# Performance work log

Measured on AMD Instinct MI355X. Metric: run time of the kernel, lower is better.

## Reference

```python
import jax, jax.numpy as jnp
import numpy as np

# dims
N, E, B, T = 1024, 8192, 4, 8          # nodes, edges, batch, time steps
IN, HID, H, NCLASS = 64, 64, 4, 7      # in_dim, nhidden, heads, nclass
K = N - NCLASS + 1                     # output-head conv width
NEG, EPS = 0.2, 1e-5


def setup_inputs() -> dict:
    key = jax.random.key(0)
    ks = jax.random.split(key, 24)
    p = lambda i, shape: jax.random.normal(ks[i], shape, jnp.float32) * 0.05
    inputs = jax.random.normal(ks[0], (B, IN, T, N), jnp.float32)
    src = jax.random.randint(ks[1], (E,), 0, N, jnp.int32)
    dst = jnp.repeat(jnp.arange(N, dtype=jnp.int32), E // N)  # every node has in-degree 8
    return {
        "inputs": inputs, "src": src, "dst": dst,
        "W0": p(2, (H * HID, IN)), "al0": p(3, (H, HID)), "ar0": p(4, (H, HID)),
        "W1": p(5, (H * HID, H * HID)), "al1": p(6, (H, HID)), "ar1": p(7, (H, HID)),
        "W2": p(8, (H * 1, H * HID)), "al2": p(9, (H, 1)), "ar2": p(10, (H, 1)),
        "Wres2": p(11, (H * 1, H * HID)),
        # Outputlayer
        "tc1_w": p(12, (H, H, T)), "tc1_b": p(13, (H,)),
        "ln1_g": jnp.ones((N, H), jnp.float32), "ln1_b": jnp.zeros((N, H), jnp.float32),
        "tc2_w": p(14, (1, H)), "tc2_b": p(15, (1,)),
        "ln2_g": jnp.ones((N, 1), jnp.float32), "ln2_b": jnp.zeros((N, 1), jnp.float32),
        "fc_w": p(16, (K,)), "fc_b": p(17, (1,)),
    }


def _gat_conv(h, src, dst, W, al, ar, res=None, act=None):
    # h: (N,B,T,F) -> feat: (N,B,T,H,D)
    heads, d = al.shape
    feat = (h @ W.T).reshape(N, B, T, heads, d)
    el = jnp.einsum('nbthd,hd->nbth', feat, al)
    er = jnp.einsum('nbthd,hd->nbth', feat, ar)
    e = jax.nn.leaky_relu(el[src] + er[dst], NEG)           # (E,B,T,H)
    emax = jax.ops.segment_max(e, dst, num_segments=N)
    ex = jnp.exp(e - emax[dst])
    den = jax.ops.segment_sum(ex, dst, num_segments=N)
    a = ex / den[dst]                                        # edge softmax over incoming edges
    out = jax.ops.segment_sum(feat[src] * a[..., None], dst, num_segments=N)  # (N,B,T,H,D)
    if res is not None:
        out = out + res
    if act is not None:
        out = act(out)
    return out


def reference(inputs, src, dst,
              W0, al0, ar0, W1, al1, ar1, W2, al2, ar2, Wres2,
              tc1_w, tc1_b, ln1_g, ln1_b, tc2_w, tc2_b, ln2_g, ln2_b, fc_w, fc_b):
    # (B,IN,T,N) -> (N,B,T,IN) : transpose(0,3).transpose(1,3)
    h = jnp.transpose(inputs.astype(jnp.float32), (3, 0, 2, 1))
    h1 = _gat_conv(h, src, dst, W0, al0, ar0, act=jax.nn.elu).reshape(N, B, T, H * HID)
    h2 = _gat_conv(h1, src, dst, W1, al1, ar1,
                   res=h1.reshape(N, B, T, H, HID), act=jax.nn.elu).reshape(N, B, T, H * HID)
    res2 = (h2 @ Wres2.T).reshape(N, B, T, H, 1)
    o = _gat_conv(h2, src, dst, W2, al2, ar2, res=res2)      # (N,B,T,H,1)
    # transpose(1,3).transpose(0,3).squeeze(-1) -> (B,H,T,N)
    x = jnp.transpose(o[..., 0], (1, 3, 2, 0))

    # Outputlayer
    # tconv1: Conv2d(H->H, kernel (T,1)) collapses time -> (B,H,N)
    x1 = jnp.einsum('oht,bhtn->bon', tc1_w, x) + tc1_b[None, :, None]
    # ln1: LayerNorm over (N,H) of (B,1,N,H)
    z = jnp.transpose(x1, (0, 2, 1))                          # (B,N,H)
    mu = z.mean(axis=(1, 2), keepdims=True)
    var = z.var(axis=(1, 2), keepdims=True)
    z = (z - mu) / jnp.sqrt(var + EPS) * ln1_g + ln1_b
    x1 = jnp.transpose(z, (0, 2, 1))                          # (B,H,N)
    # tconv2: 1x1 conv H->1 -> (B,1,N)
    x2 = jnp.einsum('oh,bhn->bon', tc2_w, x1) + tc2_b[None, :, None]
    # ln2: LayerNorm over (N,1)
    mu = x2.mean(axis=2, keepdims=True)
    var = x2.var(axis=2, keepdims=True)
    x2 = (x2 - mu) / jnp.sqrt(var + EPS) * ln2_g[:, 0] + ln2_b[:, 0]
    # fc: Conv2d(1->1, kernel (1,K)) sliding over nodes -> (B,NCLASS)
    xc = x2[:, :, None, :]                                    # (B,1,1,N) NCHW
    w = fc_w[None, None, None, :]                             # (1,1,1,K) OIHW
    out = jax.lax.conv_general_dilated(xc, w, (1, 1), 'VALID') + fc_b[None, :, None, None]
    return out[:, 0, 0, :]                                    # (B, NCLASS)
```

## Files before the change

kernel.cpp:

```cpp
#include <hip/hip_runtime.h>
#include <math.h>

#define NEGS 0.2f
#define EPSF 1e-5f

typedef short s16x8 __attribute__((ext_vector_type(8)));
typedef float f32x4 __attribute__((ext_vector_type(4)));

__device__ __forceinline__ float b2f(unsigned short u) {
  union { unsigned int i; float f; } v; v.i = ((unsigned int)u) << 16; return v.f;
}
__device__ __forceinline__ unsigned short f2b(float f) {
  union { float f; unsigned int i; } v; v.f = f;
  unsigned int x = v.i;
  return (unsigned short)((x + 0x7fffu + ((x >> 16) & 1u)) >> 16);
}

__device__ __forceinline__ float block_reduce256(float v, float* red) {
  #pragma unroll
  for (int o = 32; o > 0; o >>= 1) v += __shfl_down(v, o);
  __syncthreads();
  if ((threadIdx.x & 63) == 0) red[threadIdx.x >> 6] = v;
  __syncthreads();
  return red[0] + red[1] + red[2] + red[3];
}

__global__ __launch_bounds__(256) void k_cvt(
    const float* __restrict__ inp, const float* __restrict__ W0,
    const float* __restrict__ W1, unsigned short* __restrict__ Xb,
    unsigned short* __restrict__ W0b, unsigned short* __restrict__ W1b)
{
  __shared__ float L[64][65];
  const int tid = threadIdx.x;
  if (blockIdx.x >= 512) {
    const int j = (blockIdx.x - 512) * 256 + tid;
    W0b[j] = f2b(W0[j]);
    float4 w4 = *(const float4*)&W1[j*4];
    ushort4 o4; o4.x = f2b(w4.x); o4.y = f2b(w4.y); o4.z = f2b(w4.z); o4.w = f2b(w4.w);
    *(ushort4*)&W1b[j*4] = o4;
    return;
  }
  const int blk = blockIdx.x;
  const int n0 = (blk & 15) * 64;
  const int t  = (blk >> 4) & 7;
  const int b  = blk >> 7;
  const int nn = tid & 63, ch0 = tid >> 6;
  #pragma unroll
  for (int ch = ch0; ch < 64; ch += 4)
    L[ch][nn] = inp[((size_t)(b*64 + ch)*8 + t)*1024 + n0 + nn];
  __syncthreads();
  const int r = tid >> 2, ck = tid & 3;
  s16x8 o0, o1;
  #pragma unroll
  for (int i = 0; i < 8; ++i) o0[i] = (short)f2b(L[ck*16 + i][r]);
  #pragma unroll
  for (int i = 0; i < 8; ++i) o1[i] = (short)f2b(L[ck*16 + 8 + i][r]);
  const int row = (n0 + r)*32 + b*8 + t;
  *(s16x8*)&Xb[(size_t)row*64 + ck*16]     = o0;
  *(s16x8*)&Xb[(size_t)row*64 + ck*16 + 8] = o1;
}

template<int KD>
__global__ __launch_bounds__(256) void k_feat_mfma(
    const unsigned short* __restrict__ X, const unsigned short* __restrict__ Wb,
    const float* __restrict__ al, const float* __restrict__ ar,
    unsigned short* __restrict__ feat, float* __restrict__ el, float* __restrict__ er)
{
  __shared__ __align__(16) unsigned short Lb[64*256];
  const int tid  = threadIdx.x;
  const int w    = tid >> 6;
  const int lane = tid & 63;
  const int n16  = lane & 15;
  const int q    = lane >> 4;
  const int r0   = blockIdx.x * 64;

  f32x4 acc[4][4];
  #pragma unroll
  for (int rt = 0; rt < 4; ++rt)
    #pragma unroll
    for (int ct = 0; ct < 4; ++ct) acc[rt][ct] = (f32x4){0.f,0.f,0.f,0.f};

  #pragma unroll
  for (int kc = 0; kc < KD/32; ++kc) {
    s16x8 af[4], bf[4];
    #pragma unroll
    for (int rt = 0; rt < 4; ++rt)
      af[rt] = *(const s16x8*)&X[(size_t)(r0 + rt*16 + n16)*KD + kc*32 + q*8];
    #pragma unroll
    for (int ct = 0; ct < 4; ++ct)
      bf[ct] = *(const s16x8*)&Wb[(size_t)((w*4 + ct)*16 + n16)*KD + kc*32 + q*8];
    #pragma unroll
    for (int rt = 0; rt < 4; ++rt)
      #pragma unroll
      for (int ct = 0; ct < 4; ++ct)
        acc[rt][ct] = __builtin_amdgcn_mfma_f32_16x16x32_bf16(af[rt], bf[ct], acc[rt][ct], 0, 0, 0);
  }

  float alv[4], arv[4];
  #pragma unroll
  for (int ct = 0; ct < 4; ++ct) {
    alv[ct] = al[w*64 + ct*16 + n16];
    arv[ct] = ar[w*64 + ct*16 + n16];
  }
  #pragma unroll
  for (int rt = 0; rt < 4; ++rt) {
    #pragma unroll
    for (int reg = 0; reg < 4; ++reg) {
      float pl = acc[rt][0][reg]*alv[0] + acc[rt][1][reg]*alv[1]
               + acc[rt][2][reg]*alv[2] + acc[rt][3][reg]*alv[3];
      float pr = acc[rt][0][reg]*arv[0] + acc[rt][1][reg]*arv[1]
               + acc[rt][2][reg]*arv[2] + acc[rt][3][reg]*arv[3];
      #pragma unroll
      for (int o = 1; o < 16; o <<= 1) { pl += __shfl_xor(pl, o); pr += __shfl_xor(pr, o); }
      if (n16 == 0) {
        int r = r0 + rt*16 + q*4 + reg;
        el[r*4 + w] = pl;
        er[r*4 + w] = pr;
      }
    }
  }

  #pragma unroll
  for (int rt = 0; rt < 4; ++rt)
    #pragma unroll
    for (int ct = 0; ct < 4; ++ct)
      #pragma unroll
      for (int reg = 0; reg < 4; ++reg)
        Lb[(rt*16 + q*4 + reg)*256 + w*64 + ct*16 + n16] = f2b(acc[rt][ct][reg]);
  __syncthreads();
  #pragma unroll
  for (int i = 0; i < 8; ++i) {
    int u = tid + i*256;
    int row = u >> 5, off = (u & 31) * 8;
    *(s16x8*)&feat[(size_t)(r0 + row)*256 + off] = *(const s16x8*)&Lb[row*256 + off];
  }
}

__global__ __launch_bounds__(256) void k_agg0_feat1(
    const unsigned short* __restrict__ feat0, const float* __restrict__ el0,
    const float* __restrict__ er0, const int* __restrict__ src,
    const unsigned short* __restrict__ W1b, const float* __restrict__ al,
    const float* __restrict__ ar, unsigned short* __restrict__ h1b,
    unsigned short* __restrict__ feat1, float* __restrict__ el1, float* __restrict__ er1)
{
  __shared__ float wsm[8][4][8][4];
  __shared__ int   ssm[8];
  __shared__ __align__(16) unsigned short smbuf[32*264];
  unsigned short (*At)[264] = (unsigned short(*)[264])smbuf;
  unsigned short *Lb = smbuf;
  const int tid = threadIdx.x;
  const int n   = blockIdx.x;
  if (tid < 8) ssm[tid] = src[n*8 + tid];
  __syncthreads();
  if (tid < 128) {
    const int h = tid & 3, t = (tid >> 2) & 7, b = tid >> 5;
    const int rn = n*32 + b*8 + t;
    const float erv = er0[rn*4 + h];
    float e[8]; float m = -1e30f;
    #pragma unroll
    for (int j = 0; j < 8; ++j) {
      float v = el0[(ssm[j]*32 + b*8 + t)*4 + h] + erv;
      v = v >= 0.f ? v : NEGS * v;
      e[j] = v; m = fmaxf(m, v);
    }
    float den = 0.f;
    #pragma unroll
    for (int j = 0; j < 8; ++j) { e[j] = __expf(e[j] - m); den += e[j]; }
    const float inv = 1.f / den;
    #pragma unroll
    for (int j = 0; j < 8; ++j) wsm[j][b][t][h] = e[j] * inv;
  }
  __syncthreads();
  {
    const int hw2 = tid >> 5;
    const int l5  = tid & 31;
    const int c0  = l5 * 8;
    const int hh  = l5 >> 3;
    #pragma unroll 1
    for (int pass = 0; pass < 4; ++pass) {
      const int row = pass*8 + hw2;
      const int bb = row >> 3, tt = row & 7;
      float a[8] = {0.f,0.f,0.f,0.f,0.f,0.f,0.f,0.f};
      #pragma unroll
      for (int j = 0; j < 8; ++j) {
        const int rs = ssm[j]*32 + row;
        s16x8 v = *(const s16x8*)&feat0[(size_t)rs*256 + c0];
        const float wj = wsm[j][bb][tt][hh];
        #pragma unroll
        for (int i = 0; i < 8; ++i) a[i] = fmaf(wj, b2f((unsigned short)v[i]), a[i]);
      }
      s16x8 o;
      #pragma unroll
      for (int i = 0; i < 8; ++i) {
        float x = a[i] > 0.f ? a[i] : expm1f(a[i]);
        o[i] = (short)f2b(x);
      }
      *(s16x8*)&At[row][c0] = o;
      *(s16x8*)&h1b[(size_t)(n*32 + row)*256 + c0] = o;
    }
  }
  __syncthreads();
  const int w    = tid >> 6;
  const int lane = tid & 63;
  const int n16  = lane & 15;
  const int q    = lane >> 4;
  const int r0   = n * 32;
  f32x4 acc[2][4];
  #pragma unroll
  for (int rt = 0; rt < 2; ++rt)
    #pragma unroll
    for (int ct = 0; ct < 4; ++ct) acc[rt][ct] = (f32x4){0.f,0.f,0.f,0.f};
  #pragma unroll
  for (int kc = 0; kc < 8; ++kc) {
    s16x8 af[2], bf[4];
    #pragma unroll
    for (int rt = 0; rt < 2; ++rt)
      af[rt] = *(const s16x8*)&At[rt*16 + n16][kc*32 + q*8];
    #pragma unroll
    for (int ct = 0; ct < 4; ++ct)
      bf[ct] = *(const s16x8*)&W1b[(size_t)((w*4 + ct)*16 + n16)*256 + kc*32 + q*8];
    #pragma unroll
    for (int rt = 0; rt < 2; ++rt)
      #pragma unroll
      for (int ct = 0; ct < 4; ++ct)
        acc[rt][ct] = __builtin_amdgcn_mfma_f32_16x16x32_bf16(af[rt], bf[ct], acc[rt][ct], 0, 0, 0);
  }
  float alv[4], arv[4];
  #pragma unroll
  for (int ct = 0; ct < 4; ++ct) {
    alv[ct] = al[w*64 + ct*16 + n16];
    arv[ct] = ar[w*64 + ct*16 + n16];
  }
  #pragma unroll
  for (int rt = 0; rt < 2; ++rt) {
    #pragma unroll
    for (int reg = 0; reg < 4; ++reg) {
      float pl = acc[rt][0][reg]*alv[0] + acc[rt][1][reg]*alv[1]
               + acc[rt][2][reg]*alv[2] + acc[rt][3][reg]*alv[3];
      float pr = acc[rt][0][reg]*arv[0] + acc[rt][1][reg]*arv[1]
               + acc[rt][2][reg]*arv[2] + acc[rt][3][reg]*arv[3];
      #pragma unroll
      for (int o = 1; o < 16; o <<= 1) { pl += __shfl_xor(pl, o); pr += __shfl_xor(pr, o); }
      if (n16 == 0) {
        int r = r0 + rt*16 + q*4 + reg;
        el1[r*4 + w] = pl;
        er1[r*4 + w] = pr;
      }
    }
  }
  __syncthreads();
  #pragma unroll
  for (int rt = 0; rt < 2; ++rt)
    #pragma unroll
    for (int ct = 0; ct < 4; ++ct)
      #pragma unroll
      for (int reg = 0; reg < 4; ++reg)
        Lb[(rt*16 + q*4 + reg)*256 + w*64 + ct*16 + n16] = f2b(acc[rt][ct][reg]);
  __syncthreads();
  #pragma unroll
  for (int i = 0; i < 4; ++i) {
    int u = tid + i*256;
    int row = u >> 5, off = (u & 31) * 8;
    *(s16x8*)&feat1[(size_t)(r0 + row)*256 + off] = *(const s16x8*)&Lb[row*256 + off];
  }
}

__global__ __launch_bounds__(256) void k_agg1_proj(
    const unsigned short* __restrict__ feat1, const float* __restrict__ el,
    const float* __restrict__ er, const int* __restrict__ src,
    const unsigned short* __restrict__ h1b, const float* __restrict__ W2,
    const float* __restrict__ Wres2, float* __restrict__ feat2, float* __restrict__ res2)
{
  __shared__ float wsm[8][4][8][4];
  __shared__ int   ssm[8];
  __shared__ __align__(16) float Wp[8][256];
  const int tid = threadIdx.x;
  const int n   = blockIdx.x;
  if (tid < 8) ssm[tid] = src[n*8 + tid];
  for (int j2 = tid; j2 < 2048; j2 += 256) {
    int o = j2 >> 8, k = j2 & 255;
    Wp[o][k] = (o < 4) ? W2[o*256 + k] : Wres2[(o-4)*256 + k];
  }
  __syncthreads();
  if (tid < 128) {
    const int h = tid & 3, t = (tid >> 2) & 7, b = tid >> 5;
    const int rn = n*32 + b*8 + t;
    const float erv = er[rn*4 + h];
    float e[8]; float m = -1e30f;
    #pragma unroll
    for (int j = 0; j < 8; ++j) {
      float v = el[(ssm[j]*32 + b*8 + t)*4 + h] + erv;
      v = v >= 0.f ? v : NEGS * v;
      e[j] = v; m = fmaxf(m, v);
    }
    float den = 0.f;
    #pragma unroll
    for (int j = 0; j < 8; ++j) { e[j] = __expf(e[j] - m); den += e[j]; }
    const float inv = 1.f / den;
    #pragma unroll
    for (int j = 0; j < 8; ++j) wsm[j][b][t][h] = e[j] * inv;
  }
  __syncthreads();
  const int hw2 = tid >> 5;
  const int l5  = tid & 31;
  const int c0  = l5 * 8;
  const int hh  = l5 >> 3;
  #pragma unroll 1
  for (int pass = 0; pass < 4; ++pass) {
    const int row = pass*8 + hw2;
    const int bb = row >> 3, tt = row & 7;
    const int rn = n*32 + row;
    float a[8] = {0.f,0.f,0.f,0.f,0.f,0.f,0.f,0.f};
    #pragma unroll
    for (int j = 0; j < 8; ++j) {
      const int rs = ssm[j]*32 + row;
      s16x8 v = *(const s16x8*)&feat1[(size_t)rs*256 + c0];
      const float wj = wsm[j][bb][tt][hh];
      #pragma unroll
      for (int i = 0; i < 8; ++i) a[i] = fmaf(wj, b2f((unsigned short)v[i]), a[i]);
    }
    s16x8 rr = *(const s16x8*)&h1b[(size_t)rn*256 + c0];
    #pragma unroll
    for (int i = 0; i < 8; ++i) {
      float x = a[i] + b2f((unsigned short)rr[i]);
      a[i] = x > 0.f ? x : expm1f(x);
    }
    #pragma unroll
    for (int o = 0; o < 8; ++o) {
      float4 wa = *(const float4*)&Wp[o][c0];
      float4 wb = *(const float4*)&Wp[o][c0 + 4];
      float p = a[0]*wa.x + a[1]*wa.y + a[2]*wa.z + a[3]*wa.w
              + a[4]*wb.x + a[5]*wb.y + a[6]*wb.z + a[7]*wb.w;
      #pragma unroll
      for (int off = 1; off < 32; off <<= 1) p += __shfl_xor(p, off);
      if (l5 == 0) {
        if (o < 4) feat2[rn*4 + o] = p;
        else       res2[rn*4 + (o-4)] = p;
      }
    }
  }
}

__global__ __launch_bounds__(128) void k_agg2(
    const float* __restrict__ feat2, const float* __restrict__ res2,
    const int* __restrict__ src, const float* __restrict__ al2,
    const float* __restrict__ ar2, const float* __restrict__ tc1w,
    const float* __restrict__ tc1b, float* __restrict__ x1)
{
  __shared__ float os[4][8][4];
  const int n = blockIdx.x;
  const int tid = threadIdx.x;
  const int b = tid >> 5, t = (tid >> 2) & 7, h = tid & 3;
  const int rn = n*32 + b*8 + t;
  const float av = al2[h], rv = ar2[h];
  const float erv = feat2[rn*4 + h] * rv;
  float f[8], e[8]; float m = -1e30f;
  #pragma unroll
  for (int j = 0; j < 8; ++j) {
    int s_ = src[n*8 + j];
    f[j] = feat2[(s_*32 + b*8 + t)*4 + h];
    float v = f[j]*av + erv;
    v = v >= 0.f ? v : NEGS * v;
    e[j] = v; m = fmaxf(m, v);
  }
  float den = 0.f, num = 0.f;
  #pragma unroll
  for (int j = 0; j < 8; ++j) { float ex = __expf(e[j]-m); den += ex; num = fmaf(ex, f[j], num); }
  os[b][t][h] = num/den + res2[rn*4 + h];
  __syncthreads();
  if (tid < 16) {
    int b2 = tid >> 2, o2 = tid & 3;
    float acc = tc1b[o2];
    #pragma unroll
    for (int hh = 0; hh < 4; ++hh)
      #pragma unroll
      for (int tt = 0; tt < 8; ++tt)
        acc = fmaf(tc1w[(o2*4 + hh)*8 + tt], os[b2][tt][hh], acc);
    x1[(b2*4 + o2)*1024 + n] = acc;
  }
}

__global__ __launch_bounds__(256) void k_final(
    const float* __restrict__ x1, const float* __restrict__ ln1g,
    const float* __restrict__ ln1b, const float* __restrict__ tc2w,
    const float* __restrict__ tc2b, const float* __restrict__ ln2g,
    const float* __restrict__ ln2b, const float* __restrict__ fcw,
    const float* __restrict__ fcb, float* __restrict__ out)
{
  __shared__ float red[4];
  __shared__ float x2s[1024];
  const int b = blockIdx.x;
  const int tid = threadIdx.x;
  float s = 0.f, q = 0.f;
  for (int j = tid; j < 4096; j += 256) {
    float v = x1[b*4096 + j];
    s += v; q += v*v;
  }
  float S = block_reduce256(s, red);
  float Q = block_reduce256(q, red);
  float mu  = S * (1.f/4096.f);
  float var = Q * (1.f/4096.f) - mu*mu;
  float inv = rsqrtf(var + EPSF);
  float tb = tc2b[0];
  float s2 = 0.f, q2 = 0.f;
  for (int nn = tid; nn < 1024; nn += 256) {
    float acc = tb;
    #pragma unroll
    for (int h = 0; h < 4; ++h) {
      float z = (x1[b*4096 + h*1024 + nn] - mu) * inv * ln1g[nn*4 + h] + ln1b[nn*4 + h];
      acc = fmaf(tc2w[h], z, acc);
    }
    x2s[nn] = acc;
    s2 += acc; q2 += acc*acc;
  }
  float S2 = block_reduce256(s2, red);
  float Q2 = block_reduce256(q2, red);
  float mu2  = S2 * (1.f/1024.f);
  float inv2 = rsqrtf(Q2 * (1.f/1024.f) - mu2*mu2 + EPSF);
  __syncthreads();
  for (int nn = tid; nn < 1024; nn += 256)
    x2s[nn] = (x2s[nn] - mu2) * inv2 * ln2g[nn] + ln2b[nn];
  __syncthreads();
  for (int c = 0; c < 7; ++c) {
    float p = 0.f;
    for (int k = tid; k < 1018; k += 256) p = fmaf(x2s[c + k], fcw[k], p);
    float P = block_reduce256(p, red);
    if (tid == 0) out[b*7 + c] = P + fcb[0];
  }
}

extern "C" void kernel_launch(void* const* d_in, const int* in_sizes, int n_in,
                              void* d_out, int out_size, void* d_ws, size_t ws_size,
                              hipStream_t stream)
{
  const float* inp  = (const float*)d_in[0];
  const int*   src  = (const int*)  d_in[1];
  const float* W0   = (const float*)d_in[3];
  const float* al0  = (const float*)d_in[4];
  const float* ar0  = (const float*)d_in[5];
  const float* W1   = (const float*)d_in[6];
  const float* al1  = (const float*)d_in[7];
  const float* ar1  = (const float*)d_in[8];
  const float* W2   = (const float*)d_in[9];
  const float* al2  = (const float*)d_in[10];
  const float* ar2  = (const float*)d_in[11];
  const float* Wr2  = (const float*)d_in[12];
  const float* tc1w = (const float*)d_in[13];
  const float* tc1b = (const float*)d_in[14];
  const float* ln1g = (const float*)d_in[15];
  const float* ln1b = (const float*)d_in[16];
  const float* tc2w = (const float*)d_in[17];
  const float* tc2b = (const float*)d_in[18];
  const float* ln2g = (const float*)d_in[19];
  const float* ln2b = (const float*)d_in[20];
  const float* fcw  = (const float*)d_in[21];
  const float* fcb  = (const float*)d_in[22];
  float* out = (float*)d_out;

  unsigned short* Xb     = (unsigned short*)d_ws;
  unsigned short* W0b    = Xb     + 2097152;
  unsigned short* W1b    = W0b    + 16384;
  unsigned short* featb0 = W1b    + 65536;
  unsigned short* featb1 = featb0 + 8388608;
  unsigned short* h1b    = featb1 + 8388608;
  float* el0   = (float*)(h1b + 8388608);
  float* er0   = el0   + 131072;
  float* el1   = er0   + 131072;
  float* er1   = el1   + 131072;
  float* feat2 = er1   + 131072;
  float* res2  = feat2 + 131072;
  float* x1    = res2  + 131072;

  k_cvt<<<dim3(576), dim3(256), 0, stream>>>(inp, W0, W1, Xb, W0b, W1b);
  k_feat_mfma<64><<<dim3(512), dim3(256), 0, stream>>>(Xb, W0b, al0, ar0, featb0, el0, er0);
  k_agg0_feat1<<<dim3(1024), dim3(256), 0, stream>>>(featb0, el0, er0, src, W1b, al1, ar1,
                                                     h1b, featb1, el1, er1);
  k_agg1_proj<<<dim3(1024), dim3(256), 0, stream>>>(featb1, el1, er1, src, h1b, W2, Wr2,
                                                    feat2, res2);
  k_agg2<<<dim3(1024), dim3(128), 0, stream>>>(feat2, res2, src, al2, ar2, tc1w, tc1b, x1);
  k_final<<<dim3(4), dim3(256), 0, stream>>>(x1, ln1g, ln1b, tc2w, tc2b, ln2g, ln2b, fcw, fcb, out);
}
```

Measured before the change: 198.9 us.

## Fuse input conversion into layer-0 MFMA, double-row gather, widen final block

Merges the bf16 conversion kernel with the first GAT projection, so each block converts W0 and its input tile straight into shared memory and the Xb/W0b round trip through global memory disappears. The aggregation kernels now process two rows per pass, issuing all 16 gathers up front to expose more memory-level parallelism, and they get launch_bounds occupancy hints. The final kernel uses 1024 threads so each thread handles one node. In exchange, every block re-converts the full W0 (256x64), which adds redundant work and LDS traffic, and the larger unrolled gather raises register pressure.

```diff
diff --git a/kernel.cpp b/kernel.cpp
--- a/kernel.cpp
+++ b/kernel.cpp
@@ -16,86 +16,82 @@
   return (unsigned short)((x + 0x7fffu + ((x >> 16) & 1u)) >> 16);
 }
 
-__device__ __forceinline__ float block_reduce256(float v, float* red) {
+__device__ __forceinline__ float block_reduce1024(float v, float* red) {
   #pragma unroll
   for (int o = 32; o > 0; o >>= 1) v += __shfl_down(v, o);
   __syncthreads();
   if ((threadIdx.x & 63) == 0) red[threadIdx.x >> 6] = v;
   __syncthreads();
-  return red[0] + red[1] + red[2] + red[3];
-}
-
-__global__ __launch_bounds__(256) void k_cvt(
+  float s = 0.f;
+  #pragma unroll
+  for (int i = 0; i < 16; ++i) s += red[i];
+  return s;
+}
+
+__global__ __launch_bounds__(256) void k_feat0(
     const float* __restrict__ inp, const float* __restrict__ W0,
-    const float* __restrict__ W1, unsigned short* __restrict__ Xb,
-    unsigned short* __restrict__ W0b, unsigned short* __restrict__ W1b)
-{
-  __shared__ float L[64][65];
+    const float* __restrict__ W1, const float* __restrict__ al,
+    const float* __restrict__ ar, unsigned short* __restrict__ feat,
+    float* __restrict__ el, float* __restrict__ er,
+    unsigned short* __restrict__ W1b)
+{
   const int tid = threadIdx.x;
   if (blockIdx.x >= 512) {
     const int j = (blockIdx.x - 512) * 256 + tid;
-    W0b[j] = f2b(W0[j]);
     float4 w4 = *(const float4*)&W1[j*4];
-    ushort4 o4; o4.x = f2b(w4.x); o4.y = f2b(w4.y); o4.z = f2b(w4.z); o4.w = f2b(w4.w);
+    ushort4 o4; o4.x=f2b(w4.x); o4.y=f2b(w4.y); o4.z=f2b(w4.z); o4.w=f2b(w4.w);
     *(ushort4*)&W1b[j*4] = o4;
     return;
   }
-  const int blk = blockIdx.x;
-  const int n0 = (blk & 15) * 64;
-  const int t  = (blk >> 4) & 7;
-  const int b  = blk >> 7;
-  const int nn = tid & 63, ch0 = tid >> 6;
-  #pragma unroll
-  for (int ch = ch0; ch < 64; ch += 4)
-    L[ch][nn] = inp[((size_t)(b*64 + ch)*8 + t)*1024 + n0 + nn];
-  __syncthreads();
-  const int r = tid >> 2, ck = tid & 3;
-  s16x8 o0, o1;
-  #pragma unroll
-  for (int i = 0; i < 8; ++i) o0[i] = (short)f2b(L[ck*16 + i][r]);
-  #pragma unroll
-  for (int i = 0; i < 8; ++i) o1[i] = (short)f2b(L[ck*16 + 8 + i][r]);
-  const int row = (n0 + r)*32 + b*8 + t;
-  *(s16x8*)&Xb[(size_t)row*64 + ck*16]     = o0;
-  *(s16x8*)&Xb[(size_t)row*64 + ck*16 + 8] = o1;
-}
-
-template<int KD>
-__global__ __launch_bounds__(256) void k_feat_mfma(
-    const unsigned short* __restrict__ X, const unsigned short* __restrict__ Wb,
-    const float* __restrict__ al, const float* __restrict__ ar,
-    unsigned short* __restrict__ feat, float* __restrict__ el, float* __restrict__ er)
-{
-  __shared__ __align__(16) unsigned short Lb[64*256];
-  const int tid  = threadIdx.x;
+  __shared__ __align__(16) unsigned short Wl[256][72];
+  __shared__ __align__(16) unsigned short At[64][72];
+  const int bt = blockIdx.x & 31;
+  const int n0 = (blockIdx.x >> 5) * 64;
+  const int b  = bt >> 3, t = bt & 7;
+  #pragma unroll
+  for (int i = 0; i < 32; ++i) {
+    int e = tid + i*256;
+    float2 w2 = *(const float2*)&W0[e*2];
+    unsigned int pk = ((unsigned int)f2b(w2.y) << 16) | (unsigned int)f2b(w2.x);
+    *(unsigned int*)&At[0][0];
+    *(unsigned int*)&Wl[(e*2) >> 6][(e*2) & 63] = pk;
+  }
+  {
+    const int nn = tid & 63, cg = tid >> 6;
+    #pragma unroll
+    for (int c2 = 0; c2 < 8; ++c2) {
+      int ch = (cg*8 + c2) * 2;
+      float vx = inp[((size_t)(b*64 + ch  )*8 + t)*1024 + n0 + nn];
+      float vy = inp[((size_t)(b*64 + ch+1)*8 + t)*1024 + n0 + nn];
+      unsigned int pk = ((unsigned int)f2b(vy) << 16) | (unsigned int)f2b(vx);
+      *(unsigned int*)&At[nn][ch] = pk;
+    }
+  }
+  __syncthreads();
   const int w    = tid >> 6;
   const int lane = tid & 63;
   const int n16  = lane & 15;
   const int q    = lane >> 4;
-  const int r0   = blockIdx.x * 64;
-
   f32x4 acc[4][4];
   #pragma unroll
   for (int rt = 0; rt < 4; ++rt)
     #pragma unroll
     for (int ct = 0; ct < 4; ++ct) acc[rt][ct] = (f32x4){0.f,0.f,0.f,0.f};
-
-  #pragma unroll
-  for (int kc = 0; kc < KD/32; ++kc) {
+  #pragma unroll
+  for (int kc = 0; kc < 2; ++kc) {
     s16x8 af[4], bf[4];
     #pragma unroll
     for (int rt = 0; rt < 4; ++rt)
-      af[rt] = *(const s16x8*)&X[(size_t)(r0 + rt*16 + n16)*KD + kc*32 + q*8];
+      af[rt] = *(const s16x8*)&At[rt*16 + n16][kc*32 + q*8];
     #pragma unroll
     for (int ct = 0; ct < 4; ++ct)
-      bf[ct] = *(const s16x8*)&Wb[(size_t)((w*4 + ct)*16 + n16)*KD + kc*32 + q*8];
+      bf[ct] = *(const s16x8*)&Wl[(w*4 + ct)*16 + n16][kc*32 + q*8];
     #pragma unroll
     for (int rt = 0; rt < 4; ++rt)
       #pragma unroll
       for (int ct = 0; ct < 4; ++ct)
         acc[rt][ct] = __builtin_amdgcn_mfma_f32_16x16x32_bf16(af[rt], bf[ct], acc[rt][ct], 0, 0, 0);
   }
-
   float alv[4], arv[4];
   #pragma unroll
   for (int ct = 0; ct < 4; ++ct) {
@@ -113,13 +109,14 @@
       #pragma unroll
       for (int o = 1; o < 16; o <<= 1) { pl += __shfl_xor(pl, o); pr += __shfl_xor(pr, o); }
       if (n16 == 0) {
-        int r = r0 + rt*16 + q*4 + reg;
+        int r = (n0 + rt*16 + q*4 + reg)*32 + bt;
         el[r*4 + w] = pl;
         er[r*4 + w] = pr;
       }
     }
   }
-
+  __syncthreads();
+  unsigned short* Lb = &Wl[0][0];
   #pragma unroll
   for (int rt = 0; rt < 4; ++rt)
     #pragma unroll
@@ -131,19 +128,19 @@
   #pragma unroll
   for (int i = 0; i < 8; ++i) {
     int u = tid + i*256;
-    int row = u >> 5, off = (u & 31) * 8;
-    *(s16x8*)&feat[(size_t)(r0 + row)*256 + off] = *(const s16x8*)&Lb[row*256 + off];
-  }
-}
-
-__global__ __launch_bounds__(256) void k_agg0_feat1(
+    int m = u >> 5, off = (u & 31) * 8;
+    *(s16x8*)&feat[(size_t)((n0 + m)*32 + bt)*256 + off] = *(const s16x8*)&Lb[m*256 + off];
+  }
+}
+
+__global__ __launch_bounds__(256, 4) void k_agg0_feat1(
     const unsigned short* __restrict__ feat0, const float* __restrict__ el0,
     const float* __restrict__ er0, const int* __restrict__ src,
     const unsigned short* __restrict__ W1b, const float* __restrict__ al,
     const float* __restrict__ ar, unsigned short* __restrict__ h1b,
     unsigned short* __restrict__ feat1, float* __restrict__ el1, float* __restrict__ er1)
 {
-  __shared__ float wsm[8][4][8][4];
+  __shared__ float wsm[8][32][4];
   __shared__ int   ssm[8];
   __shared__ __align__(16) unsigned short smbuf[32*264];
   unsigned short (*At)[264] = (unsigned short(*)[264])smbuf;
@@ -153,50 +150,57 @@
   if (tid < 8) ssm[tid] = src[n*8 + tid];
   __syncthreads();
   if (tid < 128) {
-    const int h = tid & 3, t = (tid >> 2) & 7, b = tid >> 5;
-    const int rn = n*32 + b*8 + t;
+    const int m = tid >> 2, h = tid & 3;
+    const int rn = n*32 + m;
     const float erv = er0[rn*4 + h];
-    float e[8]; float m = -1e30f;
+    float e[8]; float mx = -1e30f;
     #pragma unroll
     for (int j = 0; j < 8; ++j) {
-      float v = el0[(ssm[j]*32 + b*8 + t)*4 + h] + erv;
+      float v = el0[(ssm[j]*32 + m)*4 + h] + erv;
       v = v >= 0.f ? v : NEGS * v;
-      e[j] = v; m = fmaxf(m, v);
+      e[j] = v; mx = fmaxf(mx, v);
     }
     float den = 0.f;
     #pragma unroll
-    for (int j = 0; j < 8; ++j) { e[j] = __expf(e[j] - m); den += e[j]; }
+    for (int j = 0; j < 8; ++j) { e[j] = __expf(e[j] - mx); den += e[j]; }
     const float inv = 1.f / den;
     #pragma unroll
-    for (int j = 0; j < 8; ++j) wsm[j][b][t][h] = e[j] * inv;
+    for (int j = 0; j < 8; ++j) wsm[j][m][h] = e[j] * inv;
   }
   __syncthreads();
   {
-    const int hw2 = tid >> 5;
-    const int l5  = tid & 31;
-    const int c0  = l5 * 8;
-    const int hh  = l5 >> 3;
-    #pragma unroll 1
-    for (int pass = 0; pass < 4; ++pass) {
-      const int row = pass*8 + hw2;
-      const int bb = row >> 3, tt = row & 7;
-      float a[8] = {0.f,0.f,0.f,0.f,0.f,0.f,0.f,0.f};
+    const int hw2 = tid >> 5, l5 = tid & 31;
+    const int c0 = l5 * 8, hh = l5 >> 3;
+    #pragma unroll
+    for (int p2 = 0; p2 < 2; ++p2) {
+      const int mA = p2*16 + hw2, mB = mA + 8;
+      s16x8 vA[8], vB[8];
       #pragma unroll
       for (int j = 0; j < 8; ++j) {
-        const int rs = ssm[j]*32 + row;
-        s16x8 v = *(const s16x8*)&feat0[(size_t)rs*256 + c0];
-        const float wj = wsm[j][bb][tt][hh];
+        vA[j] = *(const s16x8*)&feat0[(size_t)(ssm[j]*32 + mA)*256 + c0];
+        vB[j] = *(const s16x8*)&feat0[(size_t)(ssm[j]*32 + mB)*256 + c0];
+      }
+      float aA[8] = {0,0,0,0,0,0,0,0}, aB[8] = {0,0,0,0,0,0,0,0};
+      #pragma unroll
+      for (int j = 0; j < 8; ++j) {
+        const float wA = wsm[j][mA][hh], wB = wsm[j][mB][hh];
         #pragma unroll
-        for (int i = 0; i < 8; ++i) a[i] = fmaf(wj, b2f((unsigned short)v[i]), a[i]);
-      }
-      s16x8 o;
+        for (int i = 0; i < 8; ++i) {
+          aA[i] = fmaf(wA, b2f((unsigned short)vA[j][i]), aA[i]);
+          aB[i] = fmaf(wB, b2f((unsigned short)vB[j][i]), aB[i]);
+        }
+      }
+      s16x8 oA, oB;
       #pragma unroll
       for (int i = 0; i < 8; ++i) {
-        float x = a[i] > 0.f ? a[i] : expm1f(a[i]);
-        o[i] = (short)f2b(x);
-      }
-      *(s16x8*)&At[row][c0] = o;
-      *(s16x8*)&h1b[(size_t)(n*32 + row)*256 + c0] = o;
+        float xA = aA[i] > 0.f ? aA[i] : expm1f(aA[i]);
+        float xB = aB[i] > 0.f ? aB[i] : expm1f(aB[i]);
+        oA[i] = (short)f2b(xA); oB[i] = (short)f2b(xB);
+      }
+      *(s16x8*)&At[mA][c0] = oA;
+      *(s16x8*)&At[mB][c0] = oB;
+      *(s16x8*)&h1b[(size_t)(n*32 + mA)*256 + c0] = oA;
+      *(s16x8*)&h1b[(size_t)(n*32 + mB)*256 + c0] = oB;
     }
   }
   __syncthreads();
@@ -265,13 +269,13 @@
   }
 }
 
-__global__ __launch_bounds__(256) void k_agg1_proj(
+__global__ __launch_bounds__(256, 4) void k_agg1_proj(
     const unsigned short* __restrict__ feat1, const float* __restrict__ el,
     const float* __restrict__ er, const int* __restrict__ src,
     const unsigned short* __restrict__ h1b, const float* __restrict__ W2,
     const float* __restrict__ Wres2, float* __restrict__ feat2, float* __restrict__ res2)
 {
-  __shared__ float wsm[8][4][8][4];
+  __shared__ float wsm[8][32][4];
   __shared__ int   ssm[8];
   __shared__ __align__(16) float Wp[8][256];
   const int tid = threadIdx.x;
@@ -283,59 +287,71 @@
   }
   __syncthreads();
   if (tid < 128) {
-    const int h = tid & 3, t = (tid >> 2) & 7, b = tid >> 5;
-    const int rn = n*32 + b*8 + t;
+    const int m = tid >> 2, h = tid & 3;
+    const int rn = n*32 + m;
     const float erv = er[rn*4 + h];
-    float e[8]; float m = -1e30f;
+    float e[8]; float mx = -1e30f;
     #pragma unroll
     for (int j = 0; j < 8; ++j) {
-      float v = el[(ssm[j]*32 + b*8 + t)*4 + h] + erv;
+      float v = el[(ssm[j]*32 + m)*4 + h] + erv;
       v = v >= 0.f ? v : NEGS * v;
-      e[j] = v; m = fmaxf(m, v);
+      e[j] = v; mx = fmaxf(mx, v);
     }
     float den = 0.f;
     #pragma unroll
-    for (int j = 0; j < 8; ++j) { e[j] = __expf(e[j] - m); den += e[j]; }
+    for (int j = 0; j < 8; ++j) { e[j] = __expf(e[j] - mx); den += e[j]; }
     const float inv = 1.f / den;
     #pragma unroll
-    for (int j = 0; j < 8; ++j) wsm[j][b][t][h] = e[j] * inv;
-  }
-  __syncthreads();
-  const int hw2 = tid >> 5;
-  const int l5  = tid & 31;
-  const int c0  = l5 * 8;
-  const int hh  = l5 >> 3;
-  #pragma unroll 1
-  for (int pass = 0; pass < 4; ++pass) {
-    const int row = pass*8 + hw2;
-    const int bb = row >> 3, tt = row & 7;
-    const int rn = n*32 + row;
-    float a[8] = {0.f,0.f,0.f,0.f,0.f,0.f,0.f,0.f};
+    for (int j = 0; j < 8; ++j) wsm[j][m][h] = e[j] * inv;
+  }
+  __syncthreads();
+  const int hw2 = tid >> 5, l5 = tid & 31;
+  const int c0 = l5 * 8, hh = l5 >> 3;
+  #pragma unroll
+  for (int p2 = 0; p2 < 2; ++p2) {
+    const int mA = p2*16 + hw2, mB = mA + 8;
+    const int rnA = n*32 + mA, rnB = n*32 + mB;
+    s16x8 vA[8], vB[8], rrA, rrB;
+    rrA = *(const s16x8*)&h1b[(size_t)rnA*256 + c0];
+    rrB = *(const s16x8*)&h1b[(size_t)rnB*256 + c0];
     #pragma unroll
     for (int j = 0; j < 8; ++j) {
-      const int rs = ssm[j]*32 + row;
-      s16x8 v = *(const s16x8*)&feat1[(size_t)rs*256 + c0];
-      const float wj = wsm[j][bb][tt][hh];
-      #pragma unroll
-      for (int i = 0; i < 8; ++i) a[i] = fmaf(wj, b2f((unsigned short)v[i]), a[i]);
-    }
-    s16x8 rr = *(const s16x8*)&h1b[(size_t)rn*256 + c0];
+      vA[j] = *(const s16x8*)&feat1[(size_t)(ssm[j]*32 + mA)*256 + c0];
+      vB[j] = *(const s16x8*)&feat1[(size_t)(ssm[j]*32 + mB)*256 + c0];
+    }
+    float aA[8] = {0,0,0,0,0,0,0,0}, aB[8] = {0,0,0,0,0,0,0,0};
+    #pragma unroll
+    for (int j = 0; j < 8; ++j) {
+      const float wA = wsm[j][mA][hh], wB = wsm[j][mB][hh];
+      #pragma unroll
+      for (int i = 0; i < 8; ++i) {
+        aA[i] = fmaf(wA, b2f((unsigned short)vA[j][i]), aA[i]);
+        aB[i] = fmaf(wB, b2f((unsigned short)vB[j][i]), aB[i]);
+      }
+    }
     #pragma unroll
     for (int i = 0; i < 8; ++i) {
-      float x = a[i] + b2f((unsigned short)rr[i]);
-      a[i] = x > 0.f ? x : expm1f(x);
+      float xA = aA[i] + b2f((unsigned short)rrA[i]);
+      float xB = aB[i] + b2f((unsigned short)rrB[i]);
+      aA[i] = xA > 0.f ? xA : expm1f(xA);
+      aB[i] = xB > 0.f ? xB : expm1f(xB);
     }
     #pragma unroll
     for (int o = 0; o < 8; ++o) {
       float4 wa = *(const float4*)&Wp[o][c0];
       float4 wb = *(const float4*)&Wp[o][c0 + 4];
-      float p = a[0]*wa.x + a[1]*wa.y + a[2]*wa.z + a[3]*wa.w
-              + a[4]*wb.x + a[5]*wb.y + a[6]*wb.z + a[7]*wb.w;
-      #pragma unroll
-      for (int off = 1; off < 32; off <<= 1) p += __shfl_xor(p, off);
+      float pA = aA[0]*wa.x + aA[1]*wa.y + aA[2]*wa.z + aA[3]*wa.w
+               + aA[4]*wb.x + aA[5]*wb.y + aA[6]*wb.z + aA[7]*wb.w;
+      float pB = aB[0]*wa.x + aB[1]*wa.y + aB[2]*wa.z + aB[3]*wa.w
+               + aB[4]*wb.x + aB[5]*wb.y + aB[6]*wb.z + aB[7]*wb.w;
+      #pragma unroll
+      for (int off = 1; off < 32; off <<= 1) {
+        pA += __shfl_xor(pA, off);
+        pB += __shfl_xor(pB, off);
+      }
       if (l5 == 0) {
-        if (o < 4) feat2[rn*4 + o] = p;
-        else       res2[rn*4 + (o-4)] = p;
+        if (o < 4) { feat2[rnA*4 + o] = pA; feat2[rnB*4 + o] = pB; }
+        else       { res2[rnA*4 + (o-4)] = pA; res2[rnB*4 + (o-4)] = pB; }
       }
     }
   }
@@ -380,51 +396,44 @@
   }
 }
 
-__global__ __launch_bounds__(256) void k_final(
+__global__ __launch_bounds__(1024) void k_final(
     const float* __restrict__ x1, const float* __restrict__ ln1g,
     const float* __restrict__ ln1b, const float* __restrict__ tc2w,
     const float* __restrict__ tc2b, const float* __restrict__ ln2g,
     const float* __restrict__ ln2b, const float* __restrict__ fcw,
     const float* __restrict__ fcb, float* __restrict__ out)
 {
-  __shared__ float red[4];
+  __shared__ float red[16];
   __shared__ float x2s[1024];
   const int b = blockIdx.x;
   const int tid = threadIdx.x;
   float s = 0.f, q = 0.f;
-  for (int j = tid; j < 4096; j += 256) {
+  for (int j = tid; j < 4096; j += 1024) {
     float v = x1[b*4096 + j];
     s += v; q += v*v;
   }
-  float S = block_reduce256(s, red);
-  float Q = block_reduce256(q, red);
+  float S = block_reduce1024(s, red);
+  float Q = block_reduce1024(q, red);
   float mu  = S * (1.f/4096.f);
   float var = Q * (1.f/4096.f) - mu*mu;
   float inv = rsqrtf(var + EPSF);
   float tb = tc2b[0];
-  float s2 = 0.f, q2 = 0.f;
-  for (int nn = tid; nn < 1024; nn += 256) {
-    float acc = tb;
-    #pragma unroll
-    for (int h = 0; h < 4; ++h) {
-      float z = (x1[b*4096 + h*1024 + nn] - mu) * inv * ln1g[nn*4 + h] + ln1b[nn*4 + h];
-      acc = fmaf(tc2w[h], z, acc);
-    }
-    x2s[nn] = acc;
-    s2 += acc; q2 += acc*acc;
-  }
-  float S2 = block_reduce256(s2, red);
-  float Q2 = block_reduce256(q2, red);
+  const int nn = tid;
+  float acc = tb;
+  #pragma unroll
+  for (int h = 0; h < 4; ++h) {
+    float z = (x1[b*4096 + h*1024 + nn] - mu) * inv * ln1g[nn*4 + h] + ln1b[nn*4 + h];
+    acc = fmaf(tc2w[h], z, acc);
+  }
+  float S2 = block_reduce1024(acc, red);
+  float Q2 = block_reduce1024(acc*acc, red);
   float mu2  = S2 * (1.f/1024.f);
   float inv2 = rsqrtf(Q2 * (1.f/1024.f) - mu2*mu2 + EPSF);
-  __syncthreads();
-  for (int nn = tid; nn < 1024; nn += 256)
-    x2s[nn] = (x2s[nn] - mu2) * inv2 * ln2g[nn] + ln2b[nn];
+  x2s[nn] = (acc - mu2) * inv2 * ln2g[nn] + ln2b[nn];
   __syncthreads();
   for (int c = 0; c < 7; ++c) {
-    float p = 0.f;
-    for (int k = tid; k < 1018; k += 256) p = fmaf(x2s[c + k], fcw[k], p);
-    float P = block_reduce256(p, red);
+    float p = (tid < 1018) ? x2s[c + tid] * fcw[tid] : 0.f;
+    float P = block_reduce1024(p, red);
     if (tid == 0) out[b*7 + c] = P + fcb[0];
   }
 }
@@ -457,9 +466,7 @@
   const float* fcb  = (const float*)d_in[22];
   float* out = (float*)d_out;
 
-  unsigned short* Xb     = (unsigned short*)d_ws;
-  unsigned short* W0b    = Xb     + 2097152;
-  unsigned short* W1b    = W0b    + 16384;
+  unsigned short* W1b    = (unsigned short*)d_ws;
   unsigned short* featb0 = W1b    + 65536;
   unsigned short* featb1 = featb0 + 8388608;
   unsigned short* h1b    = featb1 + 8388608;
@@ -471,12 +478,12 @@
   float* res2  = feat2 + 131072;
   float* x1    = res2  + 131072;
 
-  k_cvt<<<dim3(576), dim3(256), 0, stream>>>(inp, W0, W1, Xb, W0b, W1b);
-  k_feat_mfma<64><<<dim3(512), dim3(256), 0, stream>>>(Xb, W0b, al0, ar0, featb0, el0, er0);
+  k_feat0<<<dim3(576), dim3(256), 0, stream>>>(inp, W0, W1, al0, ar0,
+                                               featb0, el0, er0, W1b);
   k_agg0_feat1<<<dim3(1024), dim3(256), 0, stream>>>(featb0, el0, er0, src, W1b, al1, ar1,
                                                      h1b, featb1, el1, er1);
   k_agg1_proj<<<dim3(1024), dim3(256), 0, stream>>>(featb1, el1, er1, src, h1b, W2, Wr2,
                                                     feat2, res2);
   k_agg2<<<dim3(1024), dim3(128), 0, stream>>>(feat2, res2, src, al2, ar2, tc1w, tc1b, x1);
-  k_final<<<dim3(4), dim3(256), 0, stream>>>(x1, ln1g, ln1b, tc2w, tc2b, ln2g, ln2b, fcw, fcb, out);
-}
+  k_final<<<dim3(4), dim3(1024), 0, stream>>>(x1, ln1g, ln1b, tc2w, tc2b, ln2g, ln2b, fcw, fcb, out);
+}
```

After: 178.8 us. 10.1% less time.
